# Kernel optimization log

Measured on AMD Instinct MI355X. Metric: run time of the kernel, lower is better.

## Reference

```python
import jax, jax.numpy as jnp
import numpy as np

NUM_LYR = 4
HIDDEN = 64
IN_DIM = 3
EMBED = 64  # embed_dim // pnt_cond_steps


def setup_inputs() -> dict:
    key = jax.random.key(0)
    ks = jax.random.split(key, 10)
    s = 0.05
    return {
        "x": jax.random.normal(ks[0], (256, 1, 4096, IN_DIM), dtype=jnp.float32),
        "proj_in_w": jax.random.normal(ks[1], (HIDDEN, IN_DIM), dtype=jnp.float32) * s,
        "proj_in_b": jax.random.normal(ks[2], (HIDDEN,), dtype=jnp.float32) * s,
        "lyr_w": jax.random.normal(ks[3], (NUM_LYR, HIDDEN, HIDDEN), dtype=jnp.float32) * s,
        "lyr_b": jax.random.normal(ks[4], (NUM_LYR, HIDDEN), dtype=jnp.float32) * s,
        "glyr_w": jax.random.normal(ks[5], (NUM_LYR, HIDDEN, 2 * HIDDEN), dtype=jnp.float32) * s,
        "glyr_b": jax.random.normal(ks[6], (NUM_LYR, HIDDEN), dtype=jnp.float32) * s,
        "proj_out_w": jax.random.normal(ks[7], (EMBED, HIDDEN * NUM_LYR), dtype=jnp.float32) * s,
        "proj_out_b": jax.random.normal(ks[8], (EMBED,), dtype=jnp.float32) * s,
    }


def reference(x, proj_in_w, proj_in_b, lyr_w, lyr_b, glyr_w, glyr_b, proj_out_w, proj_out_b):
    b, t, l, d = x.shape  # t == pnt_cond_steps, l == num_point (no resampling)
    h = x.reshape(b * t, l, d)
    # proj_in + ReLU: [B, L, hidden]
    h = jax.nn.relu(jnp.einsum('bld,hd->blh', h, proj_in_w) + proj_in_b)
    xs = []
    for i in range(NUM_LYR):
        h = jax.nn.relu(jnp.einsum('blh,oh->blo', h, lyr_w[i]) + lyr_b[i])
        g = jnp.max(h, axis=1, keepdims=True)  # global max-pool over points
        gx = jnp.concatenate([h, jnp.broadcast_to(g, h.shape)], axis=2)  # [B, L, 2*hidden]
        h = jax.nn.relu(jnp.einsum('blc,oc->blo', gx, glyr_w[i]) + glyr_b[i])
        xs.append(h)
    feat = jnp.concatenate(xs, axis=2)  # [B, L, hidden*num_lyr]
    out = jnp.einsum('blc,ec->ble', feat, proj_out_w) + proj_out_b
    out = jnp.max(out, axis=1)  # [B, embed]
    # rearrange '(b t) d -> b (d t)'
    out = out.reshape(b, t, -1)
    out = jnp.transpose(out, (0, 2, 1)).reshape(b, -1)
    return out
```

## Files before the change

kernel.cpp:

```cpp
#include <hip/hip_runtime.h>

#define HH   64
#define BPTS 256
#define LPB  4096
#define NBAT 256
#define NPTS (NBAT * LPB)

typedef _Float16 f16x8 __attribute__((ext_vector_type(8)));
typedef float    f32x4 __attribute__((ext_vector_type(4)));

union HL { unsigned u; _Float16 f[2]; };

__device__ __forceinline__ unsigned pack_hilo(float x) {
    HL v;
    _Float16 h = (_Float16)x;
    v.f[0] = h;
    v.f[1] = (_Float16)(x - (float)h);
    return v.u;
}

__device__ __forceinline__ int swz32(int r, int c) {
    return (r << 6) | (c ^ ((r & 7) << 3) ^ (((r >> 3) & 1) << 2));
}
__device__ __forceinline__ int swzblk(int r, int m) {
    return (r << 4) | (m ^ ((r & 7) << 1) ^ ((r >> 3) & 1));
}

__device__ __forceinline__ void read_frag(const unsigned* lds, int r, int s, int g,
                                          f16x8& fh, f16x8& fl) {
    const int m0 = s * 8 + g * 2;
    uint4 q0 = *(const uint4*)&lds[swzblk(r, m0    ) << 2];
    uint4 q1 = *(const uint4*)&lds[swzblk(r, m0 + 1) << 2];
    unsigned q[8] = {q0.x, q0.y, q0.z, q0.w, q1.x, q1.y, q1.z, q1.w};
#pragma unroll
    for (int i = 0; i < 8; ++i) { HL v; v.u = q[i]; fh[i] = v.f[0]; fl[i] = v.f[1]; }
}

__device__ __forceinline__ void mfma_gemm(const unsigned* a_lds, const unsigned* w_lds,
                                          int rb, int lane, f32x4 acc[4][4]) {
    const int rA = rb + (lane & 15);
    const int cB = lane & 15;
    const int g  = lane >> 4;
#pragma unroll
    for (int s = 0; s < 2; ++s) {
        f16x8 ah[4], al[4];
#pragma unroll
        for (int rt = 0; rt < 4; ++rt)
            read_frag(a_lds, rA + 16 * rt, s, g, ah[rt], al[rt]);
#pragma unroll
        for (int ct = 0; ct < 4; ++ct) {
            f16x8 bh, bl;
            read_frag(w_lds, cB + 16 * ct, s, g, bh, bl);
#pragma unroll
            for (int rt = 0; rt < 4; ++rt) {
                acc[rt][ct] = __builtin_amdgcn_mfma_f32_16x16x32_f16(ah[rt], bh, acc[rt][ct], 0, 0, 0);
                acc[rt][ct] = __builtin_amdgcn_mfma_f32_16x16x32_f16(ah[rt], bl, acc[rt][ct], 0, 0, 0);
                acc[rt][ct] = __builtin_amdgcn_mfma_f32_16x16x32_f16(al[rt], bh, acc[rt][ct], 0, 0, 0);
            }
        }
    }
}

__device__ __forceinline__ void write_acts(unsigned* a_lds, const f32x4 t[4][4],
                                           int rb, int lane) {
    const int g = lane >> 4, cb = lane & 15;
#pragma unroll
    for (int rt = 0; rt < 4; ++rt) {
        const int r0 = rb + 16 * rt + 4 * g;
#pragma unroll
        for (int reg = 0; reg < 4; ++reg) {
            const int r = r0 + reg;
#pragma unroll
            for (int ct = 0; ct < 4; ++ct)
                a_lds[swz32(r, 16 * ct + cb)] = pack_hilo(t[rt][ct][reg]);
        }
    }
}

__device__ __forceinline__ void stage_w(unsigned* w_lds, const float* __restrict__ W,
                                        int tid, int ldw) {
    const int o = tid >> 2, k0 = (tid & 3) << 4;
    const float* wr = &W[(size_t)o * ldw + k0];
#pragma unroll
    for (int j = 0; j < 16; j += 4) {
        float4 w4 = *(const float4*)&wr[j];
        uint4 p = make_uint4(pack_hilo(w4.x), pack_hilo(w4.y),
                             pack_hilo(w4.z), pack_hilo(w4.w));
        *(uint4*)&w_lds[swzblk(o, (k0 + j) >> 2) << 2] = p;
    }
}

__device__ __forceinline__ unsigned encf(float f) {
    unsigned u = __float_as_uint(f);
    return (u & 0x80000000u) ? ~u : (u | 0x80000000u);
}
__device__ __forceinline__ float decf(unsigned u) {
    return (u & 0x80000000u) ? __uint_as_float(u ^ 0x80000000u) : __uint_as_float(~u);
}

__global__ __launch_bounds__(256) void k_init(float* gbuf, unsigned* oenc) {
    int i = blockIdx.x * 256 + threadIdx.x;
    if (i < 4 * NBAT * HH) gbuf[i] = 0.0f;
    if (i < NBAT * HH)     oenc[i] = 0x007FFFFFu;
}

__global__ __launch_bounds__(64) void k_goff(const float* __restrict__ g,
                                             const float* __restrict__ gw,
                                             const float* __restrict__ gb,
                                             float* __restrict__ goff, int li) {
    const int b = blockIdx.x, o = threadIdx.x;
    const float* gr = &g[b * HH];
    const float* wr = &gw[(size_t)li * 64 * 128 + o * 128 + 64];
    float s = gb[li * 64 + o];
#pragma unroll
    for (int k = 0; k < 64; k += 4) {
        float4 w4 = *(const float4*)&wr[k];
        float4 g4 = *(const float4*)&gr[k];
        s = fmaf(g4.x, w4.x, fmaf(g4.y, w4.y, fmaf(g4.z, w4.z, fmaf(g4.w, w4.w, s))));
    }
    goff[(size_t)b * HH + o] = s;
}

template<int NSTAGE, bool DO_OUT>
__global__ __launch_bounds__(256, 2) void k_fused(
    const float* __restrict__ x, const float* __restrict__ piw,
    const float* __restrict__ pib, const float* __restrict__ lyrw,
    const float* __restrict__ lyrb, const float* __restrict__ gw,
    const float* __restrict__ pw, const float* __restrict__ pob,
    const float* __restrict__ goffb, float* __restrict__ gmax,
    unsigned* __restrict__ oenc) {
    __shared__ unsigned a_lds[BPTS * HH];
    __shared__ unsigned w_lds[HH * HH];
    const int tid  = threadIdx.x;
    const int lane = tid & 63, wave = tid >> 6;
    const int rb   = wave << 6;
    const int pbase = blockIdx.x * BPTS;
    const int b = pbase / LPB;
    int ch4[4];
#pragma unroll
    for (int ct = 0; ct < 4; ++ct) ch4[ct] = 16 * ct + (lane & 15);

    stage_w(w_lds, lyrw, tid, 64);
    {
        const size_t pidx = (size_t)(pbase + tid) * 3;
        const float x0 = x[pidx], x1 = x[pidx + 1], x2 = x[pidx + 2];
#pragma unroll
        for (int c4 = 0; c4 < 64; c4 += 4) {
            uint4 p;
            float vv[4];
#pragma unroll
            for (int j = 0; j < 4; ++j) {
                const int o = c4 + j;
                vv[j] = fmaxf(fmaf(piw[o * 3], x0,
                              fmaf(piw[o * 3 + 1], x1,
                              fmaf(piw[o * 3 + 2], x2, pib[o]))), 0.0f);
            }
            p.x = pack_hilo(vv[0]); p.y = pack_hilo(vv[1]);
            p.z = pack_hilo(vv[2]); p.w = pack_hilo(vv[3]);
            *(uint4*)&a_lds[swzblk(tid, c4 >> 2) << 2] = p;
        }
    }
    __syncthreads();

    f32x4 acc[4][4];
#pragma unroll
    for (int rt = 0; rt < 4; ++rt)
#pragma unroll
        for (int ct = 0; ct < 4; ++ct) {
            const float bb = lyrb[ch4[ct]];
            acc[rt][ct] = (f32x4){bb, bb, bb, bb};
        }
    mfma_gemm(a_lds, w_lds, rb, lane, acc);

    f32x4 oacc[4][4];
    if (DO_OUT) {
#pragma unroll
        for (int rt = 0; rt < 4; ++rt)
#pragma unroll
            for (int ct = 0; ct < 4; ++ct) oacc[rt][ct] = (f32x4){0.f, 0.f, 0.f, 0.f};
    }

    constexpr int NITER = DO_OUT ? 4 : (NSTAGE - 1);
#pragma unroll
    for (int li = 0; li < NITER; ++li) {
#pragma unroll
        for (int rt = 0; rt < 4; ++rt)
#pragma unroll
            for (int ct = 0; ct < 4; ++ct)
#pragma unroll
                for (int r = 0; r < 4; ++r)
                    acc[rt][ct][r] = fmaxf(acc[rt][ct][r], 0.0f);

        __syncthreads();
        write_acts(a_lds, acc, rb, lane);
        stage_w(w_lds, &gw[(size_t)li * 64 * 128], tid, 128);
        __syncthreads();

        f32x4 a2[4][4];
#pragma unroll
        for (int rt = 0; rt < 4; ++rt)
#pragma unroll
            for (int ct = 0; ct < 4; ++ct) {
                const float gv = goffb[(size_t)li * NBAT * HH + (size_t)b * HH + ch4[ct]];
                a2[rt][ct] = (f32x4){gv, gv, gv, gv};
            }
        mfma_gemm(a_lds, w_lds, rb, lane, a2);
#pragma unroll
        for (int rt = 0; rt < 4; ++rt)
#pragma unroll
            for (int ct = 0; ct < 4; ++ct)
#pragma unroll
                for (int r = 0; r < 4; ++r)
                    a2[rt][ct][r] = fmaxf(a2[rt][ct][r], 0.0f);

        __syncthreads();
        write_acts(a_lds, a2, rb, lane);
        if (DO_OUT) {
            stage_w(w_lds, &pw[(size_t)li * 64], tid, 256);
            __syncthreads();
            mfma_gemm(a_lds, w_lds, rb, lane, oacc);
            if (li < 3) {
                __syncthreads();
                stage_w(w_lds, &lyrw[(size_t)(li + 1) * 4096], tid, 64);
                __syncthreads();
            }
        } else {
            stage_w(w_lds, &lyrw[(size_t)(li + 1) * 4096], tid, 64);
            __syncthreads();
        }
        if (li < 3) {
#pragma unroll
            for (int rt = 0; rt < 4; ++rt)
#pragma unroll
                for (int ct = 0; ct < 4; ++ct) {
                    const float bb = lyrb[(li + 1) * 64 + ch4[ct]];
                    acc[rt][ct] = (f32x4){bb, bb, bb, bb};
                }
            mfma_gemm(a_lds, w_lds, rb, lane, acc);
        }
    }

    float m4[4];
    if (!DO_OUT) {
#pragma unroll
        for (int ct = 0; ct < 4; ++ct) m4[ct] = 0.0f;
#pragma unroll
        for (int rt = 0; rt < 4; ++rt)
#pragma unroll
            for (int ct = 0; ct < 4; ++ct)
#pragma unroll
                for (int r = 0; r < 4; ++r)
                    m4[ct] = fmaxf(m4[ct], fmaxf(acc[rt][ct][r], 0.0f));
    } else {
#pragma unroll
        for (int ct = 0; ct < 4; ++ct) m4[ct] = -3.4e38f;
#pragma unroll
        for (int rt = 0; rt < 4; ++rt)
#pragma unroll
            for (int ct = 0; ct < 4; ++ct)
#pragma unroll
                for (int r = 0; r < 4; ++r)
                    m4[ct] = fmaxf(m4[ct], oacc[rt][ct][r]);
    }
#pragma unroll
    for (int ct = 0; ct < 4; ++ct) {
        m4[ct] = fmaxf(m4[ct], __shfl_xor(m4[ct], 16, 64));
        m4[ct] = fmaxf(m4[ct], __shfl_xor(m4[ct], 32, 64));
    }
    __syncthreads();
    float* red = (float*)w_lds;
    if ((lane >> 4) == 0)
#pragma unroll
        for (int ct = 0; ct < 4; ++ct)
            red[wave * 64 + ct * 16 + (lane & 15)] = m4[ct];
    __syncthreads();
    if (tid < 64) {
        float v = fmaxf(fmaxf(red[tid], red[64 + tid]),
                        fmaxf(red[128 + tid], red[192 + tid]));
        if (!DO_OUT)
            atomicMax((unsigned*)&gmax[b * HH + tid], __float_as_uint(v));
        else
            atomicMax(&oenc[b * HH + tid], encf(v + pob[tid]));
    }
}

__global__ __launch_bounds__(256) void k_dec(const unsigned* __restrict__ oenc,
                                             float* __restrict__ out) {
    int i = blockIdx.x * 256 + threadIdx.x;
    out[i] = decf(oenc[i]);
}

extern "C" void kernel_launch(void* const* d_in, const int* in_sizes, int n_in,
                              void* d_out, int out_size, void* d_ws, size_t ws_size,
                              hipStream_t stream) {
    const float* x    = (const float*)d_in[0];
    const float* piw  = (const float*)d_in[1];
    const float* pib  = (const float*)d_in[2];
    const float* lyrw = (const float*)d_in[3];
    const float* lyrb = (const float*)d_in[4];
    const float* gw   = (const float*)d_in[5];
    const float* gb   = (const float*)d_in[6];
    const float* pw   = (const float*)d_in[7];
    const float* pob  = (const float*)d_in[8];
    float* out = (float*)d_out;

    float* gbuf    = (float*)d_ws;
    unsigned* oenc = (unsigned*)(gbuf + 4 * NBAT * HH);
    float* goffbuf = (float*)(oenc + NBAT * HH);

    const int nblk = NPTS / BPTS;

    k_init<<<256, 256, 0, stream>>>(gbuf, oenc);

    k_fused<1, false><<<nblk, 256, 0, stream>>>(x, piw, pib, lyrw, lyrb, gw, pw, pob,
                                                goffbuf, gbuf, oenc);
    k_goff<<<NBAT, 64, 0, stream>>>(gbuf, gw, gb, goffbuf, 0);

    k_fused<2, false><<<nblk, 256, 0, stream>>>(x, piw, pib, lyrw, lyrb, gw, pw, pob,
                                                goffbuf, gbuf + NBAT * HH, oenc);
    k_goff<<<NBAT, 64, 0, stream>>>(gbuf + NBAT * HH, gw, gb, goffbuf + NBAT * HH, 1);

    k_fused<3, false><<<nblk, 256, 0, stream>>>(x, piw, pib, lyrw, lyrb, gw, pw, pob,
                                                goffbuf, gbuf + 2 * NBAT * HH, oenc);
    k_goff<<<NBAT, 64, 0, stream>>>(gbuf + 2 * NBAT * HH, gw, gb, goffbuf + 2 * NBAT * HH, 2);

    k_fused<4, false><<<nblk, 256, 0, stream>>>(x, piw, pib, lyrw, lyrb, gw, pw, pob,
                                                goffbuf, gbuf + 3 * NBAT * HH, oenc);
    k_goff<<<NBAT, 64, 0, stream>>>(gbuf + 3 * NBAT * HH, gw, gb, goffbuf + 3 * NBAT * HH, 3);

    k_fused<4, true><<<nblk, 256, 0, stream>>>(x, piw, pib, lyrw, lyrb, gw, pw, pob,
                                               goffbuf, nullptr, oenc);

    k_dec<<<(NBAT * HH) / 256, 256, 0, stream>>>(oenc, out);
}
```

Baseline: 1.022 ms.

## Split hi/lo fp16 planes in LDS and use 512-thread blocks

Activations and weights were stored as interleaved hi/lo fp16 pairs packed into 32-bit words. They now live in separate hi and lo fp16 LDS arrays with a new XOR swizzle, so MFMA fragments load directly as f16x8 vectors instead of being unpacked element by element. Blocks grow to 512 threads (8 waves, 32 rows each), which halves each wave's accumulator tiles, lowers register pressure and raises the launch-bounds occupancy target. The cost is more waves contending at each barrier and separate scalar hi/lo stores when activations are written back.

```diff
diff --git a/kernel.cpp b/kernel.cpp
--- a/kernel.cpp
+++ b/kernel.cpp
@@ -9,85 +9,81 @@
 typedef _Float16 f16x8 __attribute__((ext_vector_type(8)));
 typedef float    f32x4 __attribute__((ext_vector_type(4)));
 
-union HL { unsigned u; _Float16 f[2]; };
-
-__device__ __forceinline__ unsigned pack_hilo(float x) {
-    HL v;
-    _Float16 h = (_Float16)x;
-    v.f[0] = h;
-    v.f[1] = (_Float16)(x - (float)h);
-    return v.u;
-}
-
-__device__ __forceinline__ int swz32(int r, int c) {
-    return (r << 6) | (c ^ ((r & 7) << 3) ^ (((r >> 3) & 1) << 2));
-}
-__device__ __forceinline__ int swzblk(int r, int m) {
-    return (r << 4) | (m ^ ((r & 7) << 1) ^ ((r >> 3) & 1));
-}
-
-__device__ __forceinline__ void read_frag(const unsigned* lds, int r, int s, int g,
-                                          f16x8& fh, f16x8& fl) {
-    const int m0 = s * 8 + g * 2;
-    uint4 q0 = *(const uint4*)&lds[swzblk(r, m0    ) << 2];
-    uint4 q1 = *(const uint4*)&lds[swzblk(r, m0 + 1) << 2];
-    unsigned q[8] = {q0.x, q0.y, q0.z, q0.w, q1.x, q1.y, q1.z, q1.w};
-#pragma unroll
-    for (int i = 0; i < 8; ++i) { HL v; v.u = q[i]; fh[i] = v.f[0]; fl[i] = v.f[1]; }
-}
-
-__device__ __forceinline__ void mfma_gemm(const unsigned* a_lds, const unsigned* w_lds,
-                                          int rb, int lane, f32x4 acc[4][4]) {
+__device__ __forceinline__ int fofs(int r, int c) {
+    return (r << 6) | ((((c >> 3) ^ (r & 7))) << 3) | (c & 7);
+}
+__device__ __forceinline__ int bofs(int r, int m) {
+    return (r << 6) | ((m ^ (r & 7)) << 3);
+}
+__device__ __forceinline__ f16x8 rd8(const _Float16* p, int r, int m) {
+    return *(const f16x8*)&p[bofs(r, m)];
+}
+
+__device__ __forceinline__ void split2(float v, _Float16& h, _Float16& l) {
+    h = (_Float16)v;
+    l = (_Float16)(v - (float)h);
+}
+
+__device__ __forceinline__ void mfma_gemm(const _Float16* ah_, const _Float16* al_,
+                                          const _Float16* wh_, const _Float16* wl_,
+                                          int rb, int lane, f32x4 acc[2][4]) {
     const int rA = rb + (lane & 15);
     const int cB = lane & 15;
     const int g  = lane >> 4;
 #pragma unroll
     for (int s = 0; s < 2; ++s) {
-        f16x8 ah[4], al[4];
-#pragma unroll
-        for (int rt = 0; rt < 4; ++rt)
-            read_frag(a_lds, rA + 16 * rt, s, g, ah[rt], al[rt]);
+        const int m = s * 4 + g;
+        f16x8 Ah[2], Al[2];
+#pragma unroll
+        for (int rt = 0; rt < 2; ++rt) {
+            Ah[rt] = rd8(ah_, rA + 16 * rt, m);
+            Al[rt] = rd8(al_, rA + 16 * rt, m);
+        }
 #pragma unroll
         for (int ct = 0; ct < 4; ++ct) {
-            f16x8 bh, bl;
-            read_frag(w_lds, cB + 16 * ct, s, g, bh, bl);
-#pragma unroll
-            for (int rt = 0; rt < 4; ++rt) {
-                acc[rt][ct] = __builtin_amdgcn_mfma_f32_16x16x32_f16(ah[rt], bh, acc[rt][ct], 0, 0, 0);
-                acc[rt][ct] = __builtin_amdgcn_mfma_f32_16x16x32_f16(ah[rt], bl, acc[rt][ct], 0, 0, 0);
-                acc[rt][ct] = __builtin_amdgcn_mfma_f32_16x16x32_f16(al[rt], bh, acc[rt][ct], 0, 0, 0);
-            }
-        }
-    }
-}
-
-__device__ __forceinline__ void write_acts(unsigned* a_lds, const f32x4 t[4][4],
-                                           int rb, int lane) {
+            f16x8 Bh = rd8(wh_, cB + 16 * ct, m);
+            f16x8 Bl = rd8(wl_, cB + 16 * ct, m);
+#pragma unroll
+            for (int rt = 0; rt < 2; ++rt) {
+                acc[rt][ct] = __builtin_amdgcn_mfma_f32_16x16x32_f16(Ah[rt], Bh, acc[rt][ct], 0, 0, 0);
+                acc[rt][ct] = __builtin_amdgcn_mfma_f32_16x16x32_f16(Ah[rt], Bl, acc[rt][ct], 0, 0, 0);
+                acc[rt][ct] = __builtin_amdgcn_mfma_f32_16x16x32_f16(Al[rt], Bh, acc[rt][ct], 0, 0, 0);
+            }
+        }
+    }
+}
+
+__device__ __forceinline__ void write_acts(_Float16* hi, _Float16* lo,
+                                           const f32x4 t[2][4], int rb, int lane) {
     const int g = lane >> 4, cb = lane & 15;
 #pragma unroll
-    for (int rt = 0; rt < 4; ++rt) {
-        const int r0 = rb + 16 * rt + 4 * g;
+    for (int rt = 0; rt < 2; ++rt)
 #pragma unroll
         for (int reg = 0; reg < 4; ++reg) {
-            const int r = r0 + reg;
-#pragma unroll
-            for (int ct = 0; ct < 4; ++ct)
-                a_lds[swz32(r, 16 * ct + cb)] = pack_hilo(t[rt][ct][reg]);
-        }
-    }
-}
-
-__device__ __forceinline__ void stage_w(unsigned* w_lds, const float* __restrict__ W,
-                                        int tid, int ldw) {
-    const int o = tid >> 2, k0 = (tid & 3) << 4;
+            const int r = rb + 16 * rt + 4 * g + reg;
+#pragma unroll
+            for (int ct = 0; ct < 4; ++ct) {
+                _Float16 h, l;
+                split2(t[rt][ct][reg], h, l);
+                const int o = fofs(r, 16 * ct + cb);
+                hi[o] = h; lo[o] = l;
+            }
+        }
+}
+
+__device__ __forceinline__ void stage_w(_Float16* wh, _Float16* wl,
+                                        const float* __restrict__ W, int tid, int ldw) {
+    const int o = tid >> 3, k0 = (tid & 7) << 3;
     const float* wr = &W[(size_t)o * ldw + k0];
-#pragma unroll
-    for (int j = 0; j < 16; j += 4) {
-        float4 w4 = *(const float4*)&wr[j];
-        uint4 p = make_uint4(pack_hilo(w4.x), pack_hilo(w4.y),
-                             pack_hilo(w4.z), pack_hilo(w4.w));
-        *(uint4*)&w_lds[swzblk(o, (k0 + j) >> 2) << 2] = p;
-    }
+    float4 a = *(const float4*)wr;
+    float4 b = *(const float4*)(wr + 4);
+    float v[8] = {a.x, a.y, a.z, a.w, b.x, b.y, b.z, b.w};
+    f16x8 h, l;
+#pragma unroll
+    for (int i = 0; i < 8; ++i) { _Float16 hh, ll; split2(v[i], hh, ll); h[i] = hh; l[i] = ll; }
+    const int ofs = bofs(o, k0 >> 3);
+    *(f16x8*)&wh[ofs] = h;
+    *(f16x8*)&wl[ofs] = l;
 }
 
 __device__ __forceinline__ unsigned encf(float f) {
@@ -122,60 +118,65 @@
 }
 
 template<int NSTAGE, bool DO_OUT>
-__global__ __launch_bounds__(256, 2) void k_fused(
+__global__ __launch_bounds__(512, 4) void k_fused(
     const float* __restrict__ x, const float* __restrict__ piw,
     const float* __restrict__ pib, const float* __restrict__ lyrw,
     const float* __restrict__ lyrb, const float* __restrict__ gw,
     const float* __restrict__ pw, const float* __restrict__ pob,
     const float* __restrict__ goffb, float* __restrict__ gmax,
     unsigned* __restrict__ oenc) {
-    __shared__ unsigned a_lds[BPTS * HH];
-    __shared__ unsigned w_lds[HH * HH];
+    __shared__ __align__(16) _Float16 a_hi[BPTS * HH];
+    __shared__ __align__(16) _Float16 a_lo[BPTS * HH];
+    __shared__ __align__(16) _Float16 w_hi[HH * HH];
+    __shared__ __align__(16) _Float16 w_lo[HH * HH];
     const int tid  = threadIdx.x;
     const int lane = tid & 63, wave = tid >> 6;
-    const int rb   = wave << 6;
+    const int rb   = wave << 5;
     const int pbase = blockIdx.x * BPTS;
     const int b = pbase / LPB;
     int ch4[4];
 #pragma unroll
     for (int ct = 0; ct < 4; ++ct) ch4[ct] = 16 * ct + (lane & 15);
 
-    stage_w(w_lds, lyrw, tid, 64);
+    stage_w(w_hi, w_lo, lyrw, tid, 64);
     {
-        const size_t pidx = (size_t)(pbase + tid) * 3;
+        const int p = tid >> 1, half = tid & 1;
+        const size_t pidx = (size_t)(pbase + p) * 3;
         const float x0 = x[pidx], x1 = x[pidx + 1], x2 = x[pidx + 2];
 #pragma unroll
-        for (int c4 = 0; c4 < 64; c4 += 4) {
-            uint4 p;
-            float vv[4];
-#pragma unroll
-            for (int j = 0; j < 4; ++j) {
-                const int o = c4 + j;
-                vv[j] = fmaxf(fmaf(piw[o * 3], x0,
+        for (int j = 0; j < 4; ++j) {
+            const int o0 = half * 32 + j * 8;
+            f16x8 h, l;
+#pragma unroll
+            for (int i = 0; i < 8; ++i) {
+                const int o = o0 + i;
+                float v = fmaxf(fmaf(piw[o * 3], x0,
                               fmaf(piw[o * 3 + 1], x1,
                               fmaf(piw[o * 3 + 2], x2, pib[o]))), 0.0f);
-            }
-            p.x = pack_hilo(vv[0]); p.y = pack_hilo(vv[1]);
-            p.z = pack_hilo(vv[2]); p.w = pack_hilo(vv[3]);
-            *(uint4*)&a_lds[swzblk(tid, c4 >> 2) << 2] = p;
+                _Float16 hh, ll; split2(v, hh, ll);
+                h[i] = hh; l[i] = ll;
+            }
+            const int ofs = bofs(p, o0 >> 3);
+            *(f16x8*)&a_hi[ofs] = h;
+            *(f16x8*)&a_lo[ofs] = l;
         }
     }
     __syncthreads();
 
-    f32x4 acc[4][4];
-#pragma unroll
-    for (int rt = 0; rt < 4; ++rt)
+    f32x4 acc[2][4];
+#pragma unroll
+    for (int rt = 0; rt < 2; ++rt)
 #pragma unroll
         for (int ct = 0; ct < 4; ++ct) {
             const float bb = lyrb[ch4[ct]];
             acc[rt][ct] = (f32x4){bb, bb, bb, bb};
         }
-    mfma_gemm(a_lds, w_lds, rb, lane, acc);
-
-    f32x4 oacc[4][4];
+    mfma_gemm(a_hi, a_lo, w_hi, w_lo, rb, lane, acc);
+
+    f32x4 oacc[2][4];
     if (DO_OUT) {
 #pragma unroll
-        for (int rt = 0; rt < 4; ++rt)
+        for (int rt = 0; rt < 2; ++rt)
 #pragma unroll
             for (int ct = 0; ct < 4; ++ct) oacc[rt][ct] = (f32x4){0.f, 0.f, 0.f, 0.f};
     }
@@ -184,7 +185,7 @@
 #pragma unroll
     for (int li = 0; li < NITER; ++li) {
 #pragma unroll
-        for (int rt = 0; rt < 4; ++rt)
+        for (int rt = 0; rt < 2; ++rt)
 #pragma unroll
             for (int ct = 0; ct < 4; ++ct)
 #pragma unroll
@@ -192,21 +193,21 @@
                     acc[rt][ct][r] = fmaxf(acc[rt][ct][r], 0.0f);
 
         __syncthreads();
-        write_acts(a_lds, acc, rb, lane);
-        stage_w(w_lds, &gw[(size_t)li * 64 * 128], tid, 128);
+        write_acts(a_hi, a_lo, acc, rb, lane);
+        stage_w(w_hi, w_lo, &gw[(size_t)li * 64 * 128], tid, 128);
         __syncthreads();
 
-        f32x4 a2[4][4];
-#pragma unroll
-        for (int rt = 0; rt < 4; ++rt)
+        f32x4 a2[2][4];
+#pragma unroll
+        for (int rt = 0; rt < 2; ++rt)
 #pragma unroll
             for (int ct = 0; ct < 4; ++ct) {
                 const float gv = goffb[(size_t)li * NBAT * HH + (size_t)b * HH + ch4[ct]];
                 a2[rt][ct] = (f32x4){gv, gv, gv, gv};
             }
-        mfma_gemm(a_lds, w_lds, rb, lane, a2);
-#pragma unroll
-        for (int rt = 0; rt < 4; ++rt)
+        mfma_gemm(a_hi, a_lo, w_hi, w_lo, rb, lane, a2);
+#pragma unroll
+        for (int rt = 0; rt < 2; ++rt)
 #pragma unroll
             for (int ct = 0; ct < 4; ++ct)
 #pragma unroll
@@ -214,29 +215,29 @@
                     a2[rt][ct][r] = fmaxf(a2[rt][ct][r], 0.0f);
 
         __syncthreads();
-        write_acts(a_lds, a2, rb, lane);
+        write_acts(a_hi, a_lo, a2, rb, lane);
         if (DO_OUT) {
-            stage_w(w_lds, &pw[(size_t)li * 64], tid, 256);
+            stage_w(w_hi, w_lo, &pw[(size_t)li * 64], tid, 256);
             __syncthreads();
-            mfma_gemm(a_lds, w_lds, rb, lane, oacc);
+            mfma_gemm(a_hi, a_lo, w_hi, w_lo, rb, lane, oacc);
             if (li < 3) {
                 __syncthreads();
-                stage_w(w_lds, &lyrw[(size_t)(li + 1) * 4096], tid, 64);
+                stage_w(w_hi, w_lo, &lyrw[(size_t)(li + 1) * 4096], tid, 64);
                 __syncthreads();
             }
         } else {
-            stage_w(w_lds, &lyrw[(size_t)(li + 1) * 4096], tid, 64);
+            stage_w(w_hi, w_lo, &lyrw[(size_t)(li + 1) * 4096], tid, 64);
             __syncthreads();
         }
         if (li < 3) {
 #pragma unroll
-            for (int rt = 0; rt < 4; ++rt)
+            for (int rt = 0; rt < 2; ++rt)
 #pragma unroll
                 for (int ct = 0; ct < 4; ++ct) {
                     const float bb = lyrb[(li + 1) * 64 + ch4[ct]];
                     acc[rt][ct] = (f32x4){bb, bb, bb, bb};
                 }
-            mfma_gemm(a_lds, w_lds, rb, lane, acc);
+            mfma_gemm(a_hi, a_lo, w_hi, w_lo, rb, lane, acc);
         }
     }
 
@@ -245,7 +246,7 @@
 #pragma unroll
         for (int ct = 0; ct < 4; ++ct) m4[ct] = 0.0f;
 #pragma unroll
-        for (int rt = 0; rt < 4; ++rt)
+        for (int rt = 0; rt < 2; ++rt)
 #pragma unroll
             for (int ct = 0; ct < 4; ++ct)
 #pragma unroll
@@ -255,7 +256,7 @@
 #pragma unroll
         for (int ct = 0; ct < 4; ++ct) m4[ct] = -3.4e38f;
 #pragma unroll
-        for (int rt = 0; rt < 4; ++rt)
+        for (int rt = 0; rt < 2; ++rt)
 #pragma unroll
             for (int ct = 0; ct < 4; ++ct)
 #pragma unroll
@@ -268,15 +269,16 @@
         m4[ct] = fmaxf(m4[ct], __shfl_xor(m4[ct], 32, 64));
     }
     __syncthreads();
-    float* red = (float*)w_lds;
+    float* red = (float*)a_hi;
     if ((lane >> 4) == 0)
 #pragma unroll
         for (int ct = 0; ct < 4; ++ct)
             red[wave * 64 + ct * 16 + (lane & 15)] = m4[ct];
     __syncthreads();
     if (tid < 64) {
-        float v = fmaxf(fmaxf(red[tid], red[64 + tid]),
-                        fmaxf(red[128 + tid], red[192 + tid]));
+        float v = red[tid];
+#pragma unroll
+        for (int w = 1; w < 8; ++w) v = fmaxf(v, red[w * 64 + tid]);
         if (!DO_OUT)
             atomicMax((unsigned*)&gmax[b * HH + tid], __float_as_uint(v));
         else
@@ -312,23 +314,23 @@
 
     k_init<<<256, 256, 0, stream>>>(gbuf, oenc);
 
-    k_fused<1, false><<<nblk, 256, 0, stream>>>(x, piw, pib, lyrw, lyrb, gw, pw, pob,
+    k_fused<1, false><<<nblk, 512, 0, stream>>>(x, piw, pib, lyrw, lyrb, gw, pw, pob,
                                                 goffbuf, gbuf, oenc);
     k_goff<<<NBAT, 64, 0, stream>>>(gbuf, gw, gb, goffbuf, 0);
 
-    k_fused<2, false><<<nblk, 256, 0, stream>>>(x, piw, pib, lyrw, lyrb, gw, pw, pob,
+    k_fused<2, false><<<nblk, 512, 0, stream>>>(x, piw, pib, lyrw, lyrb, gw, pw, pob,
                                                 goffbuf, gbuf + NBAT * HH, oenc);
     k_goff<<<NBAT, 64, 0, stream>>>(gbuf + NBAT * HH, gw, gb, goffbuf + NBAT * HH, 1);
 
-    k_fused<3, false><<<nblk, 256, 0, stream>>>(x, piw, pib, lyrw, lyrb, gw, pw, pob,
+    k_fused<3, false><<<nblk, 512, 0, stream>>>(x, piw, pib, lyrw, lyrb, gw, pw, pob,
                                                 goffbuf, gbuf + 2 * NBAT * HH, oenc);
     k_goff<<<NBAT, 64, 0, stream>>>(gbuf + 2 * NBAT * HH, gw, gb, goffbuf + 2 * NBAT * HH, 2);
 
-    k_fused<4, false><<<nblk, 256, 0, stream>>>(x, piw, pib, lyrw, lyrb, gw, pw, pob,
+    k_fused<4, false><<<nblk, 512, 0, stream>>>(x, piw, pib, lyrw, lyrb, gw, pw, pob,
                                                 goffbuf, gbuf + 3 * NBAT * HH, oenc);
     k_goff<<<NBAT, 64, 0, stream>>>(gbuf + 3 * NBAT * HH, gw, gb, goffbuf + 3 * NBAT * HH, 3);
 
-    k_fused<4, true><<<nblk, 256, 0, stream>>>(x, piw, pib, lyrw, lyrb, gw, pw, pob,
+    k_fused<4, true><<<nblk, 512, 0, stream>>>(x, piw, pib, lyrw, lyrb, gw, pw, pob,
                                                goffbuf, nullptr, oenc);
 
     k_dec<<<(NBAT * HH) / 256, 256, 0, stream>>>(oenc, out);
```

Result: slower. 1.058 ms (+3.5%).
